# Kernel tuning notes

Hardware: AMD Instinct MI355X
Metric: run time of the kernel (lower is better)

Reference implementation:

```python
import jax, jax.numpy as jnp
import numpy as np

N, E = 50000, 800000
NF, HC, H, NC = 512, 64, 8, 16
NEG_SLOPE = 0.2


def setup_inputs() -> dict:
    key = jax.random.key(0)
    ks = jax.random.split(key, 10)
    x = jax.random.normal(ks[0], (N, NF), dtype=jnp.float32)
    edge_index = jax.random.randint(ks[1], (2, E), 0, N, dtype=jnp.int64)
    # layer 1 params (GATConv nf -> hc, heads=H, concat)
    w1 = jax.random.normal(ks[2], (NF, H * HC), dtype=jnp.float32) / np.sqrt(NF)
    a_src1 = jax.random.normal(ks[3], (H, HC), dtype=jnp.float32) / np.sqrt(HC)
    a_dst1 = jax.random.normal(ks[4], (H, HC), dtype=jnp.float32) / np.sqrt(HC)
    b1 = jnp.zeros((H * HC,), dtype=jnp.float32)
    # layer 2 params (GATConv hc*h -> nc, heads=1, concat=False)
    w2 = jax.random.normal(ks[5], (H * HC, NC), dtype=jnp.float32) / np.sqrt(H * HC)
    a_src2 = jax.random.normal(ks[6], (1, NC), dtype=jnp.float32) / np.sqrt(NC)
    a_dst2 = jax.random.normal(ks[7], (1, NC), dtype=jnp.float32) / np.sqrt(NC)
    b2 = jnp.zeros((NC,), dtype=jnp.float32)
    return {"x": x, "edge_index": edge_index, "w1": w1, "a_src1": a_src1,
            "a_dst1": a_dst1, "b1": b1, "w2": w2, "a_src2": a_src2,
            "a_dst2": a_dst2, "b2": b2}


def _gat_conv(x, src, dst, W, a_src, a_dst, heads, out_ch):
    # x: [N, F_in] -> h: [N, H, C]
    h = (x @ W).reshape(N, heads, out_ch)
    alpha_src = jnp.einsum('nhc,hc->nh', h, a_src)  # [N, H]
    alpha_dst = jnp.einsum('nhc,hc->nh', h, a_dst)  # [N, H]
    e = jax.nn.leaky_relu(alpha_src[src] + alpha_dst[dst], NEG_SLOPE)  # [E', H]
    # segment-wise softmax over edges grouped by destination node
    m = jax.ops.segment_max(e, dst, num_segments=N)
    ex = jnp.exp(e - m[dst])
    denom = jax.ops.segment_sum(ex, dst, num_segments=N)
    alpha = ex / denom[dst]  # [E', H]
    out = jax.ops.segment_sum(h[src] * alpha[:, :, None], dst, num_segments=N)
    return out  # [N, H, C]


def reference(x, edge_index, w1, a_src1, a_dst1, b1, w2, a_src2, a_dst2, b2):
    # add self loops (PyG GATConv default)
    loops = jnp.arange(N, dtype=edge_index.dtype)
    src = jnp.concatenate([edge_index[0], loops])
    dst = jnp.concatenate([edge_index[1], loops])
    # layer 1: heads concatenated, dropout is identity in eval mode
    emb = _gat_conv(x, src, dst, w1, a_src1, a_dst1, H, HC).reshape(N, H * HC) + b1
    h_act = jax.nn.elu(emb)
    # layer 2: single head, no concat
    logits = _gat_conv(h_act, src, dst, w2, a_src2, a_dst2, 1, NC).reshape(N, NC) + b2
    return (logits, emb)
```

## Files before the change

kernel.cpp:

```cpp
#include <hip/hip_runtime.h>
#include <math.h>

#define N_NODES 50000
#define M_PAD   50048
#define N_EDGES 800000
#define ET (N_EDGES + N_NODES)
#define NF 512
#define HC 64
#define NH 8
#define D1 512
#define NC 16
#define NEG_SLOPE 0.2f

typedef __attribute__((ext_vector_type(8))) short bf16x8;
typedef __attribute__((ext_vector_type(4))) float floatx4;

static __device__ __forceinline__ float b2f(unsigned short u) {
  union { unsigned int i; float f; } v; v.i = ((unsigned int)u) << 16; return v.f;
}
static __device__ __forceinline__ unsigned short f2b(float f) {
  union { float f; unsigned int i; } v; v.f = f;
  unsigned int r = v.i + 0x7fffu + ((v.i >> 16) & 1u);
  return (unsigned short)(r >> 16);
}

static __device__ __forceinline__ void async_cp16(const void* g, void* l) {
  __builtin_amdgcn_global_load_lds(
      (const __attribute__((address_space(1))) unsigned int*)g,
      (__attribute__((address_space(3))) unsigned int*)l, 16, 0, 0);
}

__global__ __launch_bounds__(256) void k_w1t(const float* __restrict__ w1,
                                             unsigned short* __restrict__ w1t) {
  __shared__ float t[32][33];
  int tx = threadIdx.x & 31, ty = threadIdx.x >> 5;
  int k0 = blockIdx.x * 32, n0 = blockIdx.y * 32;
  for (int r = ty; r < 32; r += 8)
    t[r][tx] = w1[(size_t)(k0 + r) * D1 + n0 + tx];
  __syncthreads();
  for (int r = ty; r < 32; r += 8)
    w1t[(size_t)(n0 + r) * NF + k0 + tx] = f2b(t[tx][r]);
}

__global__ __launch_bounds__(512) void k_gemm1f(const float* __restrict__ x,
                                                const unsigned short* __restrict__ w1t,
                                                unsigned short* __restrict__ h1b) {
  __shared__ unsigned short As[128 * 32];
  __shared__ unsigned short Bs[2][512 * 32];
  const int tid  = threadIdx.x;
  const int w    = tid >> 6;
  const int lane = tid & 63;
  const int l16  = lane & 15;
  const int quad = lane >> 4;
  const int bm   = blockIdx.x * 128;
  const int wr   = (w >> 1) * 32;
  const int wc   = (w & 1) * 256;

  const int arow = tid >> 2;
  const int acg  = tid & 3;
  const bool aval = (bm + arow) < N_NODES;
  const float* agp = x + (size_t)(bm + arow) * NF + acg * 8;

  const int bn_base = w * 16 + (lane >> 2);
  const int bko     = (lane & 3) * 8;

  floatx4 acc[2][16] = {};
  floatx4 ar0 = {0.f, 0.f, 0.f, 0.f}, ar1 = {0.f, 0.f, 0.f, 0.f};

#pragma unroll
  for (int r = 0; r < 4; ++r) {
    const int n = r * 128 + bn_base;
    async_cp16(w1t + (size_t)n * NF + bko, &Bs[0][n * 32 + bko]);
  }
  if (aval) {
    ar0 = __builtin_nontemporal_load((const floatx4*)agp);
    ar1 = __builtin_nontemporal_load((const floatx4*)(agp + 4));
  }

  for (int s = 0; s < NF / 32; ++s) {
    const int cur = s & 1;
    bf16x8 av;
    av[0] = (short)f2b(ar0[0]); av[1] = (short)f2b(ar0[1]);
    av[2] = (short)f2b(ar0[2]); av[3] = (short)f2b(ar0[3]);
    av[4] = (short)f2b(ar1[0]); av[5] = (short)f2b(ar1[1]);
    av[6] = (short)f2b(ar1[2]); av[7] = (short)f2b(ar1[3]);
    *(bf16x8*)&As[arow * 32 + acg * 8] = av;
    __syncthreads();

    if (s + 1 < NF / 32) {
      const int kk1 = (s + 1) * 32;
#pragma unroll
      for (int r = 0; r < 4; ++r) {
        const int n = r * 128 + bn_base;
        async_cp16(w1t + (size_t)n * NF + kk1 + bko, &Bs[cur ^ 1][n * 32 + bko]);
      }
      if (aval) {
        ar0 = __builtin_nontemporal_load((const floatx4*)(agp + kk1));
        ar1 = __builtin_nontemporal_load((const floatx4*)(agp + kk1 + 4));
      }
    }

    bf16x8 af0 = *(const bf16x8*)&As[(wr + l16) * 32 + quad * 8];
    bf16x8 af1 = *(const bf16x8*)&As[(wr + 16 + l16) * 32 + quad * 8];
#pragma unroll
    for (int j = 0; j < 16; ++j) {
      bf16x8 bf = *(const bf16x8*)&Bs[cur][(wc + j * 16 + l16) * 32 + quad * 8];
      acc[0][j] = __builtin_amdgcn_mfma_f32_16x16x32_bf16(af0, bf, acc[0][j], 0, 0, 0);
      acc[1][j] = __builtin_amdgcn_mfma_f32_16x16x32_bf16(af1, bf, acc[1][j], 0, 0, 0);
    }
    __syncthreads();
  }

#pragma unroll
  for (int i = 0; i < 2; ++i)
#pragma unroll
    for (int j = 0; j < 16; ++j) {
      const int col = wc + j * 16 + l16;
#pragma unroll
      for (int r = 0; r < 4; ++r) {
        const int row = bm + wr + i * 16 + quad * 4 + r;
        h1b[(size_t)row * D1 + col] = f2b(acc[i][j][r]);
      }
    }
}

__global__ void k_alphas1(const unsigned short* __restrict__ h1b,
                          const float* __restrict__ a_src,
                          const float* __restrict__ a_dst,
                          float* __restrict__ as1, float* __restrict__ ad1) {
  int i = blockIdx.x * 256 + threadIdx.x;
  if (i >= N_NODES * NH) return;
  int n = i >> 3, hd = i & 7;
  const unsigned short* hp = h1b + (size_t)n * D1 + hd * HC;
  const float* aw = a_src + hd * HC;
  const float* dw = a_dst + hd * HC;
  float s = 0.f, d = 0.f;
#pragma unroll
  for (int c = 0; c < HC; c += 8) {
    bf16x8 hv = *(const bf16x8*)&hp[c];
#pragma unroll
    for (int j = 0; j < 8; ++j) {
      float v = b2f((unsigned short)hv[j]);
      s += v * aw[c + j];
      d += v * dw[c + j];
    }
  }
  as1[i] = s; ad1[i] = d;
}

__global__ void k_degree(const int* __restrict__ ei, int* __restrict__ deg) {
  int i = blockIdx.x * 256 + threadIdx.x;
  if (i >= ET) return;
  int dst = (i < N_EDGES) ? ei[N_EDGES + i] : (i - N_EDGES);
  atomicAdd(&deg[dst], 1);
}

__global__ void k_reduce(const int* __restrict__ deg, int* __restrict__ bsums) {
  __shared__ int s[1024];
  int i = blockIdx.x * 1024 + threadIdx.x;
  s[threadIdx.x] = (i < N_NODES) ? deg[i] : 0;
  __syncthreads();
  for (int off = 512; off > 0; off >>= 1) {
    if (threadIdx.x < off) s[threadIdx.x] += s[threadIdx.x + off];
    __syncthreads();
  }
  if (threadIdx.x == 0) bsums[blockIdx.x] = s[0];
}

__global__ void k_scan_small(int* __restrict__ bsums, int nb) {
  int lane = threadIdx.x;
  int v = (lane < nb) ? bsums[lane] : 0;
  int orig = v;
  for (int off = 1; off < 64; off <<= 1) {
    int u = __shfl_up(v, off);
    if (lane >= off) v += u;
  }
  __syncthreads();
  if (lane < nb) bsums[lane] = v - orig;
}

__global__ void k_scan_final(const int* __restrict__ deg,
                             const int* __restrict__ bsums_ex,
                             int* __restrict__ rowp, int* __restrict__ pos) {
  __shared__ int s[1024];
  int i = blockIdx.x * 1024 + threadIdx.x;
  int v = (i < N_NODES) ? deg[i] : 0;
  s[threadIdx.x] = v;
  __syncthreads();
  for (int off = 1; off < 1024; off <<= 1) {
    int t = (threadIdx.x >= off) ? s[threadIdx.x - off] : 0;
    __syncthreads();
    s[threadIdx.x] += t;
    __syncthreads();
  }
  int inc = s[threadIdx.x];
  int ex  = inc - v + bsums_ex[blockIdx.x];
  if (i < N_NODES) { rowp[i] = ex; pos[i] = ex; }
  if (i == N_NODES - 1) rowp[N_NODES] = ex + v;
}

__global__ void k_scatter(const int* __restrict__ ei, int* __restrict__ pos,
                          int* __restrict__ csr) {
  int i = blockIdx.x * 256 + threadIdx.x;
  if (i >= ET) return;
  int s, d;
  if (i < N_EDGES) { s = ei[i]; d = ei[N_EDGES + i]; }
  else             { s = d = i - N_EDGES; }
  int slot = atomicAdd(&pos[d], 1);
  csr[slot] = s;
}

static __device__ __forceinline__ void ld_edge1(const unsigned short* __restrict__ h1b,
                                                const float* __restrict__ as1,
                                                int src, int head, int col,
                                                bf16x8& hv, float& al) {
  al = as1[src * NH + head];
  hv = *(const bf16x8*)&h1b[(size_t)src * D1 + col];
}

static __device__ __forceinline__ void use_edge1(const bf16x8& hv, float al, float adv,
                                                 float& den, float acc[8]) {
  float e = al + adv;
  e = (e >= 0.f) ? e : NEG_SLOPE * e;
  float wgt = __expf(e);
  den += wgt;
#pragma unroll
  for (int jj = 0; jj < 8; ++jj) acc[jj] += wgt * b2f((unsigned short)hv[jj]);
}

__global__ __launch_bounds__(256) void k_agg1(const unsigned short* __restrict__ h1b,
                                              const float* __restrict__ as1,
                                              const float* __restrict__ ad1,
                                              const int* __restrict__ rowp,
                                              const int* __restrict__ csr,
                                              const float* __restrict__ b1,
                                              float* __restrict__ emb) {
  const int wid  = threadIdx.x >> 6;
  const int lane = threadIdx.x & 63;
  const int node = blockIdx.x * 4 + wid;
  if (node >= N_NODES) return;
  const int start = rowp[node], end = rowp[node + 1];
  const int head = lane >> 3;
  const int col  = lane * 8;
  const float adv = ad1[node * NH + head];

  bf16x8 h0, h1, h2, h3;
  float  a0, a1, a2, a3;

  {
    int i0 = __builtin_nontemporal_load(&csr[start]);
    int i1 = (start + 1 < end) ? __builtin_nontemporal_load(&csr[start + 1]) : 0;
    int i2 = (start + 2 < end) ? __builtin_nontemporal_load(&csr[start + 2]) : 0;
    int i3 = (start + 3 < end) ? __builtin_nontemporal_load(&csr[start + 3]) : 0;
    ld_edge1(h1b, as1, i0, head, col, h0, a0);
    if (start + 1 < end) ld_edge1(h1b, as1, i1, head, col, h1, a1);
    if (start + 2 < end) ld_edge1(h1b, as1, i2, head, col, h2, a2);
    if (start + 3 < end) ld_edge1(h1b, as1, i3, head, col, h3, a3);
  }

  float den = 0.f;
  float acc[8] = {};
  for (int j = start; j < end; j += 4) {
    int n0 = (j + 4 < end) ? __builtin_nontemporal_load(&csr[j + 4]) : 0;
    int n1 = (j + 5 < end) ? __builtin_nontemporal_load(&csr[j + 5]) : 0;
    int n2 = (j + 6 < end) ? __builtin_nontemporal_load(&csr[j + 6]) : 0;
    int n3 = (j + 7 < end) ? __builtin_nontemporal_load(&csr[j + 7]) : 0;
    use_edge1(h0, a0, adv, den, acc);
    if (j + 4 < end) ld_edge1(h1b, as1, n0, head, col, h0, a0);
    if (j + 1 < end) use_edge1(h1, a1, adv, den, acc);
    if (j + 5 < end) ld_edge1(h1b, as1, n1, head, col, h1, a1);
    if (j + 2 < end) use_edge1(h2, a2, adv, den, acc);
    if (j + 6 < end) ld_edge1(h1b, as1, n2, head, col, h2, a2);
    if (j + 3 < end) use_edge1(h3, a3, adv, den, acc);
    if (j + 7 < end) ld_edge1(h1b, as1, n3, head, col, h3, a3);
  }
  const float rden = 1.f / den;

  const float4 bb0 = *(const float4*)&b1[col];
  const float4 bb1 = *(const float4*)&b1[col + 4];
  floatx4 o0 = {acc[0] * rden + bb0.x, acc[1] * rden + bb0.y,
                acc[2] * rden + bb0.z, acc[3] * rden + bb0.w};
  floatx4 o1 = {acc[4] * rden + bb1.x, acc[5] * rden + bb1.y,
                acc[6] * rden + bb1.z, acc[7] * rden + bb1.w};
  __builtin_nontemporal_store(o0, (floatx4*)&emb[(size_t)node * D1 + col]);
  __builtin_nontemporal_store(o1, (floatx4*)&emb[(size_t)node * D1 + col + 4]);
}

static __device__ __forceinline__ void split_bf16(float x, unsigned short& h,
                                                  unsigned short& l) {
  h = f2b(x);
  float rem = x - b2f(h);
  l = f2b(rem);
}

__global__ __launch_bounds__(256) void k_gemm2m(const float* __restrict__ emb,
                                                const float* __restrict__ W2,
                                                const float* __restrict__ a_src2,
                                                const float* __restrict__ a_dst2,
                                                float* __restrict__ h2,
                                                float* __restrict__ as2,
                                                float* __restrict__ ad2) {
  const int wv   = threadIdx.x >> 6;
  const int lane = threadIdx.x & 63;
  const int l16  = lane & 15;
  const int quad = lane >> 4;
  const int n0 = blockIdx.x * 128 + wv * 32 + l16;
  const int n1 = n0 + 16;
  const bool v0 = n0 < N_NODES, v1 = n1 < N_NODES;

  floatx4 acc0 = {0.f, 0.f, 0.f, 0.f};
  floatx4 acc1 = {0.f, 0.f, 0.f, 0.f};

  const float* e0 = emb + (size_t)n0 * D1 + quad * 8;
  const float* e1 = emb + (size_t)n1 * D1 + quad * 8;
  const float* wp = W2 + (size_t)(quad * 8) * NC + l16;

#pragma unroll 2
  for (int kk = 0; kk < D1; kk += 32) {
    bf16x8 ah, al;
#pragma unroll
    for (int j = 0; j < 8; ++j) {
      float wv2 = wp[(size_t)(kk + j) * NC];
      unsigned short h, l;
      split_bf16(wv2, h, l);
      ah[j] = (short)h; al[j] = (short)l;
    }
    bf16x8 bh0, bl0, bh1, bl1;
    {
      floatx4 pa = {0.f, 0.f, 0.f, 0.f}, pb = {0.f, 0.f, 0.f, 0.f};
      if (v0) {
        pa = __builtin_nontemporal_load((const floatx4*)&e0[kk]);
        pb = __builtin_nontemporal_load((const floatx4*)&e0[kk + 4]);
      }
      float t[8] = {pa[0], pa[1], pa[2], pa[3], pb[0], pb[1], pb[2], pb[3]};
#pragma unroll
      for (int j = 0; j < 8; ++j) {
        float xx = t[j];
        float s = (xx > 0.f) ? xx : (__expf(xx) - 1.f);
        unsigned short h, l;
        split_bf16(s, h, l);
        bh0[j] = (short)h; bl0[j] = (short)l;
      }
    }
    {
      floatx4 pa = {0.f, 0.f, 0.f, 0.f}, pb = {0.f, 0.f, 0.f, 0.f};
      if (v1) {
        pa = __builtin_nontemporal_load((const floatx4*)&e1[kk]);
        pb = __builtin_nontemporal_load((const floatx4*)&e1[kk + 4]);
      }
      float t[8] = {pa[0], pa[1], pa[2], pa[3], pb[0], pb[1], pb[2], pb[3]};
#pragma unroll
      for (int j = 0; j < 8; ++j) {
        float xx = t[j];
        float s = (xx > 0.f) ? xx : (__expf(xx) - 1.f);
        unsigned short h, l;
        split_bf16(s, h, l);
        bh1[j] = (short)h; bl1[j] = (short)l;
      }
    }
    acc0 = __builtin_amdgcn_mfma_f32_16x16x32_bf16(ah, bh0, acc0, 0, 0, 0);
    acc0 = __builtin_amdgcn_mfma_f32_16x16x32_bf16(ah, bl0, acc0, 0, 0, 0);
    acc0 = __builtin_amdgcn_mfma_f32_16x16x32_bf16(al, bh0, acc0, 0, 0, 0);
    acc1 = __builtin_amdgcn_mfma_f32_16x16x32_bf16(ah, bh1, acc1, 0, 0, 0);
    acc1 = __builtin_amdgcn_mfma_f32_16x16x32_bf16(ah, bl1, acc1, 0, 0, 0);
    acc1 = __builtin_amdgcn_mfma_f32_16x16x32_bf16(al, bh1, acc1, 0, 0, 0);
  }

  const float4 asv = ((const float4*)a_src2)[quad];
  const float4 adv = ((const float4*)a_dst2)[quad];
  float sa0 = acc0[0] * asv.x + acc0[1] * asv.y + acc0[2] * asv.z + acc0[3] * asv.w;
  float da0 = acc0[0] * adv.x + acc0[1] * adv.y + acc0[2] * adv.z + acc0[3] * adv.w;
  float sa1 = acc1[0] * asv.x + acc1[1] * asv.y + acc1[2] * asv.z + acc1[3] * asv.w;
  float da1 = acc1[0] * adv.x + acc1[1] * adv.y + acc1[2] * adv.z + acc1[3] * adv.w;
  sa0 += __shfl_xor(sa0, 16); sa0 += __shfl_xor(sa0, 32);
  da0 += __shfl_xor(da0, 16); da0 += __shfl_xor(da0, 32);
  sa1 += __shfl_xor(sa1, 16); sa1 += __shfl_xor(sa1, 32);
  da1 += __shfl_xor(da1, 16); da1 += __shfl_xor(da1, 32);

  if (v0) {
    *(float4*)&h2[(size_t)n0 * NC + quad * 4] =
        make_float4(acc0[0], acc0[1], acc0[2], acc0[3]);
    if (quad == 0) { as2[n0] = sa0; ad2[n0] = da0; }
  }
  if (v1) {
    *(float4*)&h2[(size_t)n1 * NC + quad * 4] =
        make_float4(acc1[0], acc1[1], acc1[2], acc1[3]);
    if (quad == 0) { as2[n1] = sa1; ad2[n1] = da1; }
  }
}

__global__ __launch_bounds__(256) void k_agg2(const float* __restrict__ h2,
                                              const float* __restrict__ as2,
                                              const float* __restrict__ ad2,
                                              const int* __restrict__ rowp,
                                              const int* __restrict__ csr,
                                              const float* __restrict__ b2,
                                              float* __restrict__ logits) {
  const int wid  = threadIdx.x >> 6;
  const int lane = threadIdx.x & 63;
  const int node = blockIdx.x * 4 + wid;
  if (node >= N_NODES) return;
  const int start = rowp[node], end = rowp[node + 1];
  const float adv = ad2[node];
  const int g = lane >> 4;
  const int c = lane & 15;

  int jA = start + g;
  int sA = (jA < end) ? csr[jA] : -1;
  int jB = jA + 4;
  int sB = (jB < end) ? csr[jB] : -1;
  float eA = 0.f, vA = 0.f;
  if (sA >= 0) { eA = as2[sA]; vA = h2[(size_t)sA * NC + c]; }

  float den = 0.f, acc = 0.f;
  for (int base = start; base < end; base += 4) {
    float eB = 0.f, vB = 0.f;
    if (sB >= 0) { eB = as2[sB]; vB = h2[(size_t)sB * NC + c]; }
    int jC = base + 8 + g;
    int sC = (jC < end) ? csr[jC] : -1;
    if (sA >= 0) {
      float e = eA + adv;
      e = (e >= 0.f) ? e : NEG_SLOPE * e;
      float wgt = __expf(e);
      den += wgt;
      acc += wgt * vA;
    }
    sA = sB; eA = eB; vA = vB; sB = sC;
  }
  acc += __shfl_xor(acc, 16); acc += __shfl_xor(acc, 32);
  den += __shfl_xor(den, 16); den += __shfl_xor(den, 32);
  if (lane < 16) logits[(size_t)node * NC + lane] = acc / den + b2[lane];
}

extern "C" void kernel_launch(void* const* d_in, const int* in_sizes, int n_in,
                              void* d_out, int out_size, void* d_ws, size_t ws_size,
                              hipStream_t stream) {
  const float* x      = (const float*)d_in[0];
  const int*   ei     = (const int*)d_in[1];
  const float* w1     = (const float*)d_in[2];
  const float* a_src1 = (const float*)d_in[3];
  const float* a_dst1 = (const float*)d_in[4];
  const float* b1     = (const float*)d_in[5];
  const float* w2     = (const float*)d_in[6];
  const float* a_src2 = (const float*)d_in[7];
  const float* a_dst2 = (const float*)d_in[8];
  const float* b2     = (const float*)d_in[9];

  char* w = (char*)d_ws;
  char* xb_region = w;
  w += (size_t)M_PAD * NF * 2;
  unsigned short* h1b = (unsigned short*)w; w += (size_t)M_PAD * D1 * 2;
  unsigned short* w1t = (unsigned short*)w; w += (size_t)NF * D1 * 2;
  float* as1 = (float*)w;  w += (size_t)N_NODES * NH * 4;
  float* ad1 = (float*)w;  w += (size_t)N_NODES * NH * 4;
  int* deg   = (int*)w;    w += (size_t)N_NODES * 4;
  int* rowp  = (int*)w;    w += (size_t)50064 * 4;
  int* pos   = (int*)w;    w += (size_t)N_NODES * 4;
  int* csr   = (int*)w;    w += (size_t)ET * 4;
  int* bsums = (int*)w;    w += 256;
  float* h2  = (float*)xb_region;
  float* as2 = (float*)(xb_region + (size_t)N_NODES * NC * 4);
  float* ad2 = (float*)(xb_region + (size_t)N_NODES * NC * 4 + (size_t)N_NODES * 4);

  float* logits = (float*)d_out;
  float* emb    = (float*)d_out + (size_t)N_NODES * NC;

  hipMemsetAsync(deg, 0, N_NODES * sizeof(int), stream);

  k_w1t<<<dim3(16, 16), 256, 0, stream>>>(w1, w1t);
  k_gemm1f<<<M_PAD / 128, 512, 0, stream>>>(x, w1t, h1b);
  k_alphas1<<<(N_NODES * NH + 255) / 256, 256, 0, stream>>>(h1b, a_src1, a_dst1, as1, ad1);

  k_degree<<<(ET + 255) / 256, 256, 0, stream>>>(ei, deg);
  k_reduce<<<49, 1024, 0, stream>>>(deg, bsums);
  k_scan_small<<<1, 64, 0, stream>>>(bsums, 49);
  k_scan_final<<<49, 1024, 0, stream>>>(deg, bsums, rowp, pos);
  k_scatter<<<(ET + 255) / 256, 256, 0, stream>>>(ei, pos, csr);

  k_agg1<<<(N_NODES + 3) / 4, 256, 0, stream>>>(h1b, as1, ad1, rowp, csr, b1, emb);

  k_gemm2m<<<(N_NODES + 127) / 128, 256, 0, stream>>>(emb, w2, a_src2, a_dst2, h2, as2, ad2);
  k_agg2<<<(N_NODES + 3) / 4, 256, 0, stream>>>(h2, as2, ad2, rowp, csr, b2, logits);
}
```

Before: 550.5 us.

## Fuse attention-logit dot products into GEMM epilogue and merge small preprocessing kernels

Computes the per-node, per-head source and destination attention scores directly from the GEMM accumulators, using shuffle reductions and a shared-memory staging area. This removes the separate pass that re-read the bf16 features to compute them. It also folds the weight transpose into the degree-counting kernel and merges the small bsums scan into the final scan kernel, which now uses wave shuffles. The aim is fewer launches and less memory traffic, at the cost of more epilogue work and register pressure in the GEMM. The scores are now computed from fp32 accumulators rather than rounded bf16 values, so they can differ slightly from before.

After: 526.1 us. -4.4%, faster.

```diff
diff --git a/kernel.cpp b/kernel.cpp
--- a/kernel.cpp
+++ b/kernel.cpp
@@ -30,21 +30,35 @@
       (__attribute__((address_space(3))) unsigned int*)l, 16, 0, 0);
 }
 
-__global__ __launch_bounds__(256) void k_w1t(const float* __restrict__ w1,
-                                             unsigned short* __restrict__ w1t) {
-  __shared__ float t[32][33];
-  int tx = threadIdx.x & 31, ty = threadIdx.x >> 5;
-  int k0 = blockIdx.x * 32, n0 = blockIdx.y * 32;
-  for (int r = ty; r < 32; r += 8)
-    t[r][tx] = w1[(size_t)(k0 + r) * D1 + n0 + tx];
-  __syncthreads();
-  for (int r = ty; r < 32; r += 8)
-    w1t[(size_t)(n0 + r) * NF + k0 + tx] = f2b(t[tx][r]);
+__global__ __launch_bounds__(256) void k_wdeg(const float* __restrict__ w1,
+                                              unsigned short* __restrict__ w1t,
+                                              const int* __restrict__ ei,
+                                              int* __restrict__ deg) {
+  const int b = blockIdx.x;
+  if (b < 256) {
+    __shared__ float t[32][33];
+    int tx = threadIdx.x & 31, ty = threadIdx.x >> 5;
+    int k0 = (b & 15) * 32, n0 = (b >> 4) * 32;
+    for (int r = ty; r < 32; r += 8)
+      t[r][tx] = w1[(size_t)(k0 + r) * D1 + n0 + tx];
+    __syncthreads();
+    for (int r = ty; r < 32; r += 8)
+      w1t[(size_t)(n0 + r) * NF + k0 + tx] = f2b(t[tx][r]);
+  }
+  int i = b * 256 + threadIdx.x;
+  if (i < ET) {
+    int dst = (i < N_EDGES) ? ei[N_EDGES + i] : (i - N_EDGES);
+    atomicAdd(&deg[dst], 1);
+  }
 }
 
 __global__ __launch_bounds__(512) void k_gemm1f(const float* __restrict__ x,
                                                 const unsigned short* __restrict__ w1t,
-                                                unsigned short* __restrict__ h1b) {
+                                                unsigned short* __restrict__ h1b,
+                                                const float* __restrict__ a_src1,
+                                                const float* __restrict__ a_dst1,
+                                                float* __restrict__ as1,
+                                                float* __restrict__ ad1) {
   __shared__ unsigned short As[128 * 32];
   __shared__ unsigned short Bs[2][512 * 32];
   const int tid  = threadIdx.x;
@@ -54,7 +68,8 @@
   const int quad = lane >> 4;
   const int bm   = blockIdx.x * 128;
   const int wr   = (w >> 1) * 32;
-  const int wc   = (w & 1) * 256;
+  const int half = w & 1;
+  const int wc   = half * 256;
 
   const int arow = tid >> 2;
   const int acg  = tid & 3;
@@ -122,37 +137,55 @@
         h1b[(size_t)row * D1 + col] = f2b(acc[i][j][r]);
       }
     }
-}
-
-__global__ void k_alphas1(const unsigned short* __restrict__ h1b,
-                          const float* __restrict__ a_src,
-                          const float* __restrict__ a_dst,
-                          float* __restrict__ as1, float* __restrict__ ad1) {
-  int i = blockIdx.x * 256 + threadIdx.x;
-  if (i >= N_NODES * NH) return;
-  int n = i >> 3, hd = i & 7;
-  const unsigned short* hp = h1b + (size_t)n * D1 + hd * HC;
-  const float* aw = a_src + hd * HC;
-  const float* dw = a_dst + hd * HC;
-  float s = 0.f, d = 0.f;
-#pragma unroll
-  for (int c = 0; c < HC; c += 8) {
-    bf16x8 hv = *(const bf16x8*)&hp[c];
-#pragma unroll
-    for (int j = 0; j < 8; ++j) {
-      float v = b2f((unsigned short)hv[j]);
-      s += v * aw[c + j];
-      d += v * dw[c + j];
-    }
-  }
-  as1[i] = s; ad1[i] = d;
-}
-
-__global__ void k_degree(const int* __restrict__ ei, int* __restrict__ deg) {
-  int i = blockIdx.x * 256 + threadIdx.x;
-  if (i >= ET) return;
-  int dst = (i < N_EDGES) ? ei[N_EDGES + i] : (i - N_EDGES);
-  atomicAdd(&deg[dst], 1);
+
+  float* alpS = (float*)&Bs[0][0];
+  float* alpD = alpS + 128 * 9;
+  float afs[16], ads[16];
+#pragma unroll
+  for (int j = 0; j < 16; ++j) {
+    afs[j] = a_src1[wc + j * 16 + l16];
+    ads[j] = a_dst1[wc + j * 16 + l16];
+  }
+#pragma unroll
+  for (int i = 0; i < 2; ++i)
+#pragma unroll
+    for (int r = 0; r < 4; ++r) {
+      float s0 = 0.f, s1 = 0.f, s2 = 0.f, s3 = 0.f;
+      float d0 = 0.f, d1 = 0.f, d2 = 0.f, d3 = 0.f;
+#pragma unroll
+      for (int j = 0; j < 16; ++j) {
+        float v = acc[i][j][r];
+        if ((j >> 2) == 0) { s0 += v * afs[j]; d0 += v * ads[j]; }
+        if ((j >> 2) == 1) { s1 += v * afs[j]; d1 += v * ads[j]; }
+        if ((j >> 2) == 2) { s2 += v * afs[j]; d2 += v * ads[j]; }
+        if ((j >> 2) == 3) { s3 += v * afs[j]; d3 += v * ads[j]; }
+      }
+#pragma unroll
+      for (int m = 1; m < 16; m <<= 1) {
+        s0 += __shfl_xor(s0, m); s1 += __shfl_xor(s1, m);
+        s2 += __shfl_xor(s2, m); s3 += __shfl_xor(s3, m);
+        d0 += __shfl_xor(d0, m); d1 += __shfl_xor(d1, m);
+        d2 += __shfl_xor(d2, m); d3 += __shfl_xor(d3, m);
+      }
+      if (l16 == 0) {
+        const int rl = wr + i * 16 + quad * 4 + r;
+        alpS[rl * 9 + half * 4 + 0] = s0; alpS[rl * 9 + half * 4 + 1] = s1;
+        alpS[rl * 9 + half * 4 + 2] = s2; alpS[rl * 9 + half * 4 + 3] = s3;
+        alpD[rl * 9 + half * 4 + 0] = d0; alpD[rl * 9 + half * 4 + 1] = d1;
+        alpD[rl * 9 + half * 4 + 2] = d2; alpD[rl * 9 + half * 4 + 3] = d3;
+      }
+    }
+  __syncthreads();
+#pragma unroll
+  for (int e = 0; e < 2; ++e) {
+    const int idx = tid + e * 512;
+    const int rl = idx >> 3, hd = idx & 7;
+    const int n = bm + rl;
+    if (n < N_NODES) {
+      as1[n * NH + hd] = alpS[rl * 9 + hd];
+      ad1[n * NH + hd] = alpD[rl * 9 + hd];
+    }
+  }
 }
 
 __global__ void k_reduce(const int* __restrict__ deg, int* __restrict__ bsums) {
@@ -167,34 +200,48 @@
   if (threadIdx.x == 0) bsums[blockIdx.x] = s[0];
 }
 
-__global__ void k_scan_small(int* __restrict__ bsums, int nb) {
-  int lane = threadIdx.x;
-  int v = (lane < nb) ? bsums[lane] : 0;
-  int orig = v;
+__global__ __launch_bounds__(1024) void k_scan_final(const int* __restrict__ deg,
+                                                     const int* __restrict__ bsums,
+                                                     int* __restrict__ rowp,
+                                                     int* __restrict__ pos) {
+  __shared__ int ws[16];
+  __shared__ int sprefix;
+  const int tid = threadIdx.x, bid = blockIdx.x;
+  const int lane = tid & 63, wid = tid >> 6;
+
+  if (tid < 64) {
+    int v = (tid < 49) ? bsums[tid] : 0;
+    int inc = v;
+#pragma unroll
+    for (int off = 1; off < 64; off <<= 1) {
+      int u = __shfl_up(inc, off);
+      if (tid >= off) inc += u;
+    }
+    if (tid == bid) sprefix = inc - v;
+  }
+
+  const int i = bid * 1024 + tid;
+  int v = (i < N_NODES) ? deg[i] : 0;
+  int inc = v;
+#pragma unroll
   for (int off = 1; off < 64; off <<= 1) {
-    int u = __shfl_up(v, off);
-    if (lane >= off) v += u;
-  }
+    int u = __shfl_up(inc, off);
+    if (lane >= off) inc += u;
+  }
+  if (lane == 63) ws[wid] = inc;
   __syncthreads();
-  if (lane < nb) bsums[lane] = v - orig;
-}
-
-__global__ void k_scan_final(const int* __restrict__ deg,
-                             const int* __restrict__ bsums_ex,
-                             int* __restrict__ rowp, int* __restrict__ pos) {
-  __shared__ int s[1024];
-  int i = blockIdx.x * 1024 + threadIdx.x;
-  int v = (i < N_NODES) ? deg[i] : 0;
-  s[threadIdx.x] = v;
+  if (tid < 16) {
+    int wv = ws[tid];
+    int winc = wv;
+#pragma unroll
+    for (int off = 1; off < 16; off <<= 1) {
+      int u = __shfl_up(winc, off);
+      if (tid >= off) winc += u;
+    }
+    ws[tid] = winc - wv;
+  }
   __syncthreads();
-  for (int off = 1; off < 1024; off <<= 1) {
-    int t = (threadIdx.x >= off) ? s[threadIdx.x - off] : 0;
-    __syncthreads();
-    s[threadIdx.x] += t;
-    __syncthreads();
-  }
-  int inc = s[threadIdx.x];
-  int ex  = inc - v + bsums_ex[blockIdx.x];
+  const int ex = inc - v + ws[wid] + sprefix;
   if (i < N_NODES) { rowp[i] = ex; pos[i] = ex; }
   if (i == N_NODES - 1) rowp[N_NODES] = ex + v;
 }
@@ -467,13 +514,10 @@
 
   hipMemsetAsync(deg, 0, N_NODES * sizeof(int), stream);
 
-  k_w1t<<<dim3(16, 16), 256, 0, stream>>>(w1, w1t);
-  k_gemm1f<<<M_PAD / 128, 512, 0, stream>>>(x, w1t, h1b);
-  k_alphas1<<<(N_NODES * NH + 255) / 256, 256, 0, stream>>>(h1b, a_src1, a_dst1, as1, ad1);
-
-  k_degree<<<(ET + 255) / 256, 256, 0, stream>>>(ei, deg);
+  k_wdeg<<<(ET + 255) / 256, 256, 0, stream>>>(w1, w1t, ei, deg);
+  k_gemm1f<<<M_PAD / 128, 512, 0, stream>>>(x, w1t, h1b, a_src1, a_dst1, as1, ad1);
+
   k_reduce<<<49, 1024, 0, stream>>>(deg, bsums);
-  k_scan_small<<<1, 64, 0, stream>>>(bsums, 49);
   k_scan_final<<<49, 1024, 0, stream>>>(deg, bsums, rowp, pos);
   k_scatter<<<(ET + 255) / 256, 256, 0, stream>>>(ei, pos, csr);
 
```
